# Optimization experiments

Measured on AMD Instinct MI355X. Metric: run time of the kernel, lower is better.

## Reference

```python
import jax, jax.numpy as jnp
import numpy as np

CUTOFF = 10.0
NUM_GAUSSIANS = 50
LOG2 = float(np.log(2.0))
PI = float(np.pi)


def ssp(v):
    # shifted softplus: softplus(x) - log(2)
    return jax.nn.softplus(v) - LOG2


def setup_inputs() -> dict:
    key = jax.random.key(0)
    ks = jax.random.split(key, 16)
    N, E, H, F, G, L = 10000, 320000, 128, 128, NUM_GAUSSIANS, 6
    s = 0.08  # param scale to keep activations stable over 6 layers
    return {
        "x": jax.random.randint(ks[0], (N,), 0, 100),
        "edge_index": jax.random.randint(ks[1], (2, E), 0, N),
        "edge_dist": jax.random.uniform(ks[2], (E,), jnp.float32) * CUTOFF,
        "emb": jax.random.normal(ks[3], (100, H), jnp.float32) * s,
        "mlp_w1": jax.random.normal(ks[4], (L, G, F), jnp.float32) * s,
        "mlp_b1": jnp.zeros((L, F), jnp.float32),
        "mlp_w2": jax.random.normal(ks[5], (L, F, F), jnp.float32) * s,
        "mlp_b2": jnp.zeros((L, F), jnp.float32),
        "lin1_w": jax.random.normal(ks[6], (L, H, F), jnp.float32) * s,
        "lin2_w": jax.random.normal(ks[7], (L, F, H), jnp.float32) * s,
        "lin2_b": jnp.zeros((L, H), jnp.float32),
        "lin_w": jax.random.normal(ks[8], (L, H, H), jnp.float32) * s,
        "lin_b": jnp.zeros((L, H), jnp.float32),
        "out1_w": jax.random.normal(ks[9], (H, H // 2), jnp.float32) * s,
        "out1_b": jnp.zeros((H // 2,), jnp.float32),
        "out2_w": jax.random.normal(ks[10], (H // 2, H // 2), jnp.float32) * s,
        "out2_b": jnp.zeros((H // 2,), jnp.float32),
        "ro_w": jax.random.normal(ks[11], (H // 2, 12), jnp.float32) * s,
        "ro_b": jnp.zeros((12,), jnp.float32),
    }


def reference(x, edge_index, edge_dist, emb, mlp_w1, mlp_b1, mlp_w2, mlp_b2,
              lin1_w, lin2_w, lin2_b, lin_w, lin_b,
              out1_w, out1_b, out2_w, out2_b, ro_w, ro_b):
    N = x.shape[0]
    L = mlp_w1.shape[0]
    src, dst = edge_index[0], edge_index[1]

    h = emb[x]  # [N, H]

    # Gaussian smearing of distances -> [E, G]
    offset = jnp.linspace(0.0, CUTOFF, NUM_GAUSSIANS)
    coeff = -0.5 / (offset[1] - offset[0]) ** 2
    ea = jnp.exp(coeff * (edge_dist[:, None] - offset[None, :]) ** 2)

    # cosine cutoff envelope C [E]
    C = 0.5 * (jnp.cos(edge_dist * PI / CUTOFF) + 1.0)

    for l in range(L):
        # per-edge filter: MLP(gaussian) * cutoff  -> [E, F]
        W = (ssp(ea @ mlp_w1[l] + mlp_b1[l]) @ mlp_w2[l] + mlp_b2[l]) * C[:, None]
        xf = h @ lin1_w[l]                      # [N, F] (lin1, no bias)
        msg = xf[src] * W                       # gather + elementwise [E, F]
        agg = jax.ops.segment_sum(msg, dst, num_segments=N)  # scatter-add
        conv = agg @ lin2_w[l] + lin2_b[l]      # [N, H]
        h = h + (ssp(conv) @ lin_w[l] + lin_b[l])

    t = ssp(h @ out1_w + out1_b)
    t = t @ out2_w + out2_b
    h_agg = jnp.sum(t, axis=0)                  # [H//2]
    return h_agg @ ro_w + ro_b                  # [12]
```

## Files before the change

kernel.cpp:

```cpp
#include <hip/hip_runtime.h>
#include <math.h>

#define E_NUM 320000
#define N_NUM 10000
#define NB16  (N_NUM / 16)
#define TAB   2048

typedef unsigned short ushort_t;
typedef short short8_t __attribute__((ext_vector_type(8)));
typedef float f32x4    __attribute__((ext_vector_type(4)));

#define WP_O1   294912
#define WP_O2   303104
#define WP_W1T  307200
#define WP_W2T  356352
#define WP_TOT  454656

#define HB  1250
#define PB  ((WP_TOT + 255) / 256)

#define FK_SC 625
#define FK_TB 768
#define FK_EM NB16

__device__ __forceinline__ float ssp_f(float x) {
    return fmaxf(x, 0.f) + __logf(1.f + __expf(-fabsf(x))) - 0.69314718056f;
}

__device__ __forceinline__ float bf2f(ushort_t u) {
    union { unsigned int i; float f; } v;
    v.i = ((unsigned int)u) << 16;
    return v.f;
}
__device__ __forceinline__ ushort_t f2bf(float f) {
    union { float f; unsigned int i; } v;
    v.f = f;
    unsigned int u = v.i;
    unsigned int r = (u + 0x7FFFu + ((u >> 16) & 1u)) >> 16;
    return (ushort_t)r;
}

__global__ __launch_bounds__(256) void hist_pack_kernel(const int* __restrict__ ei,
                                                        int* __restrict__ counts,
                                                        const float* __restrict__ lin2_w,
                                                        const float* __restrict__ lin_w,
                                                        const float* __restrict__ lin1_w,
                                                        const float* __restrict__ o1w,
                                                        const float* __restrict__ o2w,
                                                        const float* __restrict__ mlp_w1,
                                                        const float* __restrict__ mlp_w2,
                                                        short* __restrict__ wpack) {
    if (blockIdx.x < HB) {
        int e = blockIdx.x * 256 + threadIdx.x;
        atomicAdd(&counts[ei[E_NUM + e]], 1);
        return;
    }
    int idx = (blockIdx.x - HB) * 256 + threadIdx.x;
    const int M128 = 16384;
    if (idx < 18 * M128) {
        int g = idx / M128, r = idx % M128;
        const float* src;
        if (g < 6) src = lin2_w + g * M128;
        else if (g < 12) src = lin_w + (g - 6) * M128;
        else src = lin1_w + (g - 12) * M128;
        int j = r & 7, L = (r >> 3) & 63, ks = (r >> 9) & 3, t = r >> 11;
        int n = t * 16 + (L & 15);
        int k = ks * 32 + (L >> 4) * 8 + j;
        wpack[idx] = (short)f2bf(src[k * 128 + n]);
    } else if (idx < WP_O2) {
        int r = idx - WP_O1;
        int j = r & 7, L = (r >> 3) & 63, ks = (r >> 9) & 3, t = r >> 11;
        int n = t * 16 + (L & 15);
        int k = ks * 32 + (L >> 4) * 8 + j;
        wpack[idx] = (short)f2bf(o1w[k * 64 + n]);
    } else if (idx < WP_W1T) {
        int r = idx - WP_O2;
        int j = r & 7, L = (r >> 3) & 63, ks = (r >> 9) & 1, t = r >> 10;
        int n = t * 16 + (L & 15);
        int k = ks * 32 + (L >> 4) * 8 + j;
        wpack[idx] = (short)f2bf(o2w[k * 64 + n]);
    } else if (idx < WP_W1T + 6 * 8192 && idx >= WP_W1T) {
        int r2 = idx - WP_W1T;
        int g = r2 / 8192, r = r2 % 8192;
        int j = r & 7, L = (r >> 3) & 63, ks = (r >> 9) & 1, t = r >> 10;
        int n = t * 16 + (L & 15);
        int k = ks * 32 + (L >> 4) * 8 + j;
        float v = (k < 50) ? mlp_w1[g * 6400 + k * 128 + n] : 0.f;
        wpack[idx] = (short)f2bf(v);
    } else if (idx < WP_TOT) {
        int r2 = idx - WP_W2T;
        int g = r2 / M128, r = r2 % M128;
        int j = r & 7, L = (r >> 3) & 63, ks = (r >> 9) & 3, t = r >> 11;
        int n = t * 16 + (L & 15);
        int k = ks * 32 + (L >> 4) * 8 + j;
        wpack[idx] = (short)f2bf(mlp_w2[g * M128 + k * 128 + n]);
    }
}

__global__ __launch_bounds__(1024) void scan_kernel(const int* __restrict__ counts,
                                                    int* __restrict__ offs,
                                                    int* __restrict__ cursor) {
    __shared__ int part[1024];
    const int tid = threadIdx.x;
    const int CH = 10;
    int base = tid * CH;
    int s = 0;
    #pragma unroll
    for (int i = 0; i < CH; ++i) {
        int idx = base + i;
        if (idx < N_NUM) s += counts[idx];
    }
    part[tid] = s;
    __syncthreads();
    for (int off = 1; off < 1024; off <<= 1) {
        int v = (tid >= off) ? part[tid - off] : 0;
        __syncthreads();
        part[tid] += v;
        __syncthreads();
    }
    int run = (tid > 0) ? part[tid - 1] : 0;
    #pragma unroll
    for (int i = 0; i < CH; ++i) {
        int idx = base + i;
        if (idx < N_NUM) {
            offs[idx] = run;
            cursor[idx] = run;
            run += counts[idx];
        }
    }
    if (tid == 1023) offs[N_NUM] = part[1023];
}

__global__ __launch_bounds__(512) void front_kernel(const int* __restrict__ ei,
                                                    const float* __restrict__ dist,
                                                    int* __restrict__ cursor,
                                                    int* __restrict__ meta,
                                                    const short* __restrict__ w1t,
                                                    const float* __restrict__ mlp_b1,
                                                    const short* __restrict__ w2t,
                                                    const float* __restrict__ mlp_b2,
                                                    ushort_t* __restrict__ tabB,
                                                    const int* __restrict__ x,
                                                    const float* __restrict__ emb,
                                                    const short* __restrict__ w1p0,
                                                    float* __restrict__ h,
                                                    ushort_t* __restrict__ xf) {
    __shared__ short EA[16 * 72];
    __shared__ short HD[16 * 136];
    __shared__ int s_x[16];
    const int tid = threadIdx.x;

    if (blockIdx.x < FK_SC) {
        int e = blockIdx.x * 512 + tid;
        int d = ei[E_NUM + e];
        int pos = atomicAdd(&cursor[d], 1);
        float t = dist[e] * ((float)(TAB - 1) / 10.0f);
        int i0 = (int)(t + 0.5f);
        if (i0 > TAB - 1) i0 = TAB - 1;
        meta[pos] = (i0 << 14) | ei[e];
        return;
    }

    const int wv = tid >> 6;
    const int lane = tid & 63;
    const int m = lane & 15, q = lane >> 4;

    if (blockIdx.x < FK_SC + FK_TB) {
        const int bt = blockIdx.x - FK_SC;
        const int l = bt >> 7;
        const int r0 = (bt & 127) * 16;
        const float DG = 10.0f / (float)(TAB - 1);
        const float STEP = 10.0f / 49.0f;
        const float COEFF = -0.5f / (STEP * STEP);

        for (int i = tid; i < 16 * 64; i += 512) {
            int r = i >> 6, k = i & 63;
            float v = 0.f;
            if (k < 50) {
                float d = (float)(r0 + r) * DG;
                float t = d - (float)k * STEP;
                v = __expf(COEFF * t * t);
            }
            EA[r * 72 + k] = (short)f2bf(v);
        }
        __syncthreads();

        {
            f32x4 acc = {0.f, 0.f, 0.f, 0.f};
            #pragma unroll
            for (int ks = 0; ks < 2; ++ks) {
                short8_t a = *(const short8_t*)(EA + m * 72 + ks * 32 + q * 8);
                short8_t b = *(const short8_t*)(w1t + l * 8192 + (wv * 2 + ks) * 512 + lane * 8);
                acc = __builtin_amdgcn_mfma_f32_16x16x32_bf16(a, b, acc, 0, 0, 0);
            }
            float bv = mlp_b1[l * 128 + wv * 16 + m];
            #pragma unroll
            for (int i = 0; i < 4; ++i)
                HD[(q * 4 + i) * 136 + wv * 16 + m] = (short)f2bf(ssp_f(acc[i] + bv));
        }
        __syncthreads();

        {
            f32x4 acc = {0.f, 0.f, 0.f, 0.f};
            #pragma unroll
            for (int ks = 0; ks < 4; ++ks) {
                short8_t a = *(const short8_t*)(HD + m * 136 + ks * 32 + q * 8);
                short8_t b = *(const short8_t*)(w2t + l * 16384 + (wv * 4 + ks) * 512 + lane * 8);
                acc = __builtin_amdgcn_mfma_f32_16x16x32_bf16(a, b, acc, 0, 0, 0);
            }
            int col = wv * 16 + m;
            float bv = mlp_b2[l * 128 + col];
            ushort_t* tl = tabB + (size_t)l * TAB * 128;
            #pragma unroll
            for (int i = 0; i < 4; ++i) {
                int row = r0 + q * 4 + i;
                float d = (float)row * DG;
                float C = 0.5f * (__cosf(d * 0.31415926535f) + 1.0f);
                tl[(size_t)row * 128 + col] = f2bf((acc[i] + bv) * C);
            }
        }
        return;
    }

    {
        const int n0 = (blockIdx.x - FK_SC - FK_TB) * 16;
        if (tid < 16) s_x[tid] = x[n0 + tid];
        __syncthreads();
        {
            int r = tid >> 5;
            int c4 = (tid & 31) * 4;
            float4 v = *(const float4*)(emb + (size_t)s_x[r] * 128 + c4);
            *(float4*)(h + (size_t)(n0 + r) * 128 + c4) = v;
            short4 o;
            o.x = (short)f2bf(v.x); o.y = (short)f2bf(v.y);
            o.z = (short)f2bf(v.z); o.w = (short)f2bf(v.w);
            *(short4*)(HD + r * 136 + c4) = o;
        }
        __syncthreads();
        f32x4 acc = {0.f, 0.f, 0.f, 0.f};
        #pragma unroll
        for (int ks = 0; ks < 4; ++ks) {
            short8_t a = *(const short8_t*)(HD + m * 136 + ks * 32 + q * 8);
            short8_t b = *(const short8_t*)(w1p0 + (wv * 4 + ks) * 512 + lane * 8);
            acc = __builtin_amdgcn_mfma_f32_16x16x32_bf16(a, b, acc, 0, 0, 0);
        }
        #pragma unroll
        for (int i = 0; i < 4; ++i) {
            int grow = n0 + q * 4 + i;
            xf[(size_t)grow * 128 + wv * 16 + m] = f2bf(acc[i]);
        }
    }
}

__device__ __forceinline__ void nacc8(short8_t x, short8_t t, float* o) {
    #pragma unroll
    for (int j = 0; j < 8; ++j)
        o[j] = fmaf(bf2f((ushort_t)x[j]), bf2f((ushort_t)t[j]), o[j]);
}

template <bool LAST>
__global__ __launch_bounds__(512, 4) void layer_kernel(const int* __restrict__ offs,
                                                    const int* __restrict__ meta,
                                                    const ushort_t* __restrict__ xf,
                                                    const ushort_t* __restrict__ tabB,
                                                    const short* __restrict__ w2p,
                                                    const float* __restrict__ lin2_b,
                                                    const short* __restrict__ wlp,
                                                    const float* __restrict__ lin_b,
                                                    const short* __restrict__ w1p,
                                                    float* __restrict__ h,
                                                    ushort_t* __restrict__ xf_out,
                                                    const short* __restrict__ o1p,
                                                    const float* __restrict__ o1b,
                                                    const short* __restrict__ o2p,
                                                    const float* __restrict__ o2b,
                                                    float* __restrict__ gs) {
    __shared__ short A1[16 * 136];
    __shared__ short A2[16 * 136];
    __shared__ float P[16 * 128];
    __shared__ float red[4][64];
    const int tid = threadIdx.x;
    const int n0 = blockIdx.x * 16;
    const int wv = tid >> 6;
    const int lane = tid & 63;
    const int strm = wv >> 2;

    {
        const int qt = lane >> 4;
        const int c8 = (lane & 15) * 8;
        const int row = (wv & 3) * 4 + qt;
        const int node = n0 + row;
        int s0 = offs[node];
        int s1 = offs[node + 1];
        int mid = s0 + ((s1 - s0) >> 1);
        int e   = strm ? mid : s0;
        int end = strm ? s1  : mid;

        float accA[8] = {0.f, 0.f, 0.f, 0.f, 0.f, 0.f, 0.f, 0.f};
        float accB[8] = {0.f, 0.f, 0.f, 0.f, 0.f, 0.f, 0.f, 0.f};

        const int nb = (end - e) >> 2;
        if (nb > 0) {
            int mnxt[4] = {0, 0, 0, 0};
            short8_t xv[4], tv[4];
            {
                int mcur[4];
                #pragma unroll
                for (int u = 0; u < 4; ++u) mcur[u] = meta[e + u];
                if (nb > 1) {
                    #pragma unroll
                    for (int u = 0; u < 4; ++u) mnxt[u] = meta[e + 4 + u];
                }
                #pragma unroll
                for (int u = 0; u < 4; ++u) {
                    xv[u] = *(const short8_t*)(xf + (size_t)(mcur[u] & 0x3FFF) * 128 + c8);
                    tv[u] = *(const short8_t*)(tabB + (size_t)((unsigned)mcur[u] >> 14) * 128 + c8);
                }
            }
            for (int b = 0; b < nb - 1; ++b) {
                short8_t xn[4], tn[4];
                #pragma unroll
                for (int u = 0; u < 4; ++u) {
                    xn[u] = *(const short8_t*)(xf + (size_t)(mnxt[u] & 0x3FFF) * 128 + c8);
                    tn[u] = *(const short8_t*)(tabB + (size_t)((unsigned)mnxt[u] >> 14) * 128 + c8);
                }
                int mn2[4] = {0, 0, 0, 0};
                if (b + 2 < nb) {
                    #pragma unroll
                    for (int u = 0; u < 4; ++u) mn2[u] = meta[e + 4 * (b + 2) + u];
                }
                #pragma unroll
                for (int u = 0; u < 4; ++u)
                    nacc8(xv[u], tv[u], (u & 1) ? accB : accA);
                #pragma unroll
                for (int u = 0; u < 4; ++u) { xv[u] = xn[u]; tv[u] = tn[u]; mnxt[u] = mn2[u]; }
            }
            #pragma unroll
            for (int u = 0; u < 4; ++u)
                nacc8(xv[u], tv[u], (u & 1) ? accB : accA);
            e += nb * 4;
        }
        int rem = end - e;
        if (rem > 0) {
            int mm[4];
            #pragma unroll
            for (int u = 0; u < 4; ++u) mm[u] = meta[e + ((u < rem) ? u : 0)];
            short8_t xv[4], tv[4];
            #pragma unroll
            for (int u = 0; u < 4; ++u) {
                xv[u] = *(const short8_t*)(xf + (size_t)(mm[u] & 0x3FFF) * 128 + c8);
                tv[u] = *(const short8_t*)(tabB + (size_t)((unsigned)mm[u] >> 14) * 128 + c8);
            }
            #pragma unroll
            for (int u = 0; u < 4; ++u)
                if (u < rem) nacc8(xv[u], tv[u], (u & 1) ? accB : accA);
        }

        if (!strm) {
            #pragma unroll
            for (int j = 0; j < 8; ++j)
                P[row * 128 + c8 + j] = accA[j] + accB[j];
        }
        __syncthreads();
        if (strm) {
            short8_t out;
            #pragma unroll
            for (int j = 0; j < 8; ++j)
                out[j] = (short)f2bf(accA[j] + accB[j] + P[row * 128 + c8 + j]);
            *(short8_t*)&A1[row * 136 + c8] = out;
        }
    }
    __syncthreads();

    const int m = lane & 15, q = lane >> 4;
    const int t = wv;

    {
        f32x4 acc = {0.f, 0.f, 0.f, 0.f};
        #pragma unroll
        for (int ks = 0; ks < 4; ++ks) {
            short8_t a = *(const short8_t*)(A1 + m * 136 + ks * 32 + q * 8);
            short8_t b = *(const short8_t*)(w2p + (t * 4 + ks) * 512 + lane * 8);
            acc = __builtin_amdgcn_mfma_f32_16x16x32_bf16(a, b, acc, 0, 0, 0);
        }
        float bv = lin2_b[t * 16 + m];
        #pragma unroll
        for (int i = 0; i < 4; ++i)
            A2[(q * 4 + i) * 136 + t * 16 + m] = (short)f2bf(ssp_f(acc[i] + bv));
    }
    __syncthreads();

    {
        f32x4 acc = {0.f, 0.f, 0.f, 0.f};
        #pragma unroll
        for (int ks = 0; ks < 4; ++ks) {
            short8_t a = *(const short8_t*)(A2 + m * 136 + ks * 32 + q * 8);
            short8_t b = *(const short8_t*)(wlp + (t * 4 + ks) * 512 + lane * 8);
            acc = __builtin_amdgcn_mfma_f32_16x16x32_bf16(a, b, acc, 0, 0, 0);
        }
        float bv = lin_b[t * 16 + m];
        #pragma unroll
        for (int i = 0; i < 4; ++i) {
            int r = q * 4 + i;
            int grow = n0 + r;
            float h0 = h[(size_t)grow * 128 + t * 16 + m];
            float hn = h0 + acc[i] + bv;
            if (!LAST) h[(size_t)grow * 128 + t * 16 + m] = hn;
            A1[r * 136 + t * 16 + m] = (short)f2bf(hn);
        }
    }
    __syncthreads();

    if constexpr (!LAST) {
        f32x4 acc = {0.f, 0.f, 0.f, 0.f};
        #pragma unroll
        for (int ks = 0; ks < 4; ++ks) {
            short8_t a = *(const short8_t*)(A1 + m * 136 + ks * 32 + q * 8);
            short8_t b = *(const short8_t*)(w1p + (t * 4 + ks) * 512 + lane * 8);
            acc = __builtin_amdgcn_mfma_f32_16x16x32_bf16(a, b, acc, 0, 0, 0);
        }
        #pragma unroll
        for (int i = 0; i < 4; ++i) {
            int r = q * 4 + i;
            int grow = n0 + r;
            xf_out[(size_t)grow * 128 + t * 16 + m] = f2bf(acc[i]);
        }
    } else {
        if (wv < 4) {
            f32x4 acc = {0.f, 0.f, 0.f, 0.f};
            #pragma unroll
            for (int ks = 0; ks < 4; ++ks) {
                short8_t a = *(const short8_t*)(A1 + m * 136 + ks * 32 + q * 8);
                short8_t b = *(const short8_t*)(o1p + (wv * 4 + ks) * 512 + lane * 8);
                acc = __builtin_amdgcn_mfma_f32_16x16x32_bf16(a, b, acc, 0, 0, 0);
            }
            float bv = o1b[wv * 16 + m];
            #pragma unroll
            for (int i = 0; i < 4; ++i) {
                int r = q * 4 + i;
                A2[r * 136 + wv * 16 + m] = (short)f2bf(ssp_f(acc[i] + bv));
            }
        }
        __syncthreads();
        if (wv < 4) {
            f32x4 acc = {0.f, 0.f, 0.f, 0.f};
            #pragma unroll
            for (int ks = 0; ks < 2; ++ks) {
                short8_t a = *(const short8_t*)(A2 + m * 136 + ks * 32 + q * 8);
                short8_t b = *(const short8_t*)(o2p + (wv * 2 + ks) * 512 + lane * 8);
                acc = __builtin_amdgcn_mfma_f32_16x16x32_bf16(a, b, acc, 0, 0, 0);
            }
            float bv = o2b[wv * 16 + m];
            float part = acc[0] + acc[1] + acc[2] + acc[3] + 4.0f * bv;
            red[q][wv * 16 + m] = part;
        }
        __syncthreads();
        if (tid < 64) {
            float s = red[0][tid] + red[1][tid] + red[2][tid] + red[3][tid];
            atomicAdd(&gs[tid], s);
        }
    }
}

__global__ void final_kernel(const float* __restrict__ gs,
                             const float* __restrict__ ro_w,
                             const float* __restrict__ ro_b,
                             float* __restrict__ out) {
    int i = threadIdx.x;
    if (i < 12) {
        float s = ro_b[i];
        for (int k = 0; k < 64; ++k) s = fmaf(gs[k], ro_w[k * 12 + i], s);
        out[i] = s;
    }
}

extern "C" void kernel_launch(void* const* d_in, const int* in_sizes, int n_in,
                              void* d_out, int out_size, void* d_ws, size_t ws_size,
                              hipStream_t stream) {
    const int*   x      = (const int*)d_in[0];
    const int*   ei     = (const int*)d_in[1];
    const float* dist   = (const float*)d_in[2];
    const float* emb    = (const float*)d_in[3];
    const float* mlp_w1 = (const float*)d_in[4];
    const float* mlp_b1 = (const float*)d_in[5];
    const float* mlp_w2 = (const float*)d_in[6];
    const float* mlp_b2 = (const float*)d_in[7];
    const float* lin1_w = (const float*)d_in[8];
    const float* lin2_w = (const float*)d_in[9];
    const float* lin2_b = (const float*)d_in[10];
    const float* lin_w  = (const float*)d_in[11];
    const float* lin_b  = (const float*)d_in[12];
    const float* out1_w = (const float*)d_in[13];
    const float* out1_b = (const float*)d_in[14];
    const float* out2_w = (const float*)d_in[15];
    const float* out2_b = (const float*)d_in[16];
    const float* ro_w   = (const float*)d_in[17];
    const float* ro_b   = (const float*)d_in[18];
    float* out = (float*)d_out;

    char* base = (char*)d_ws;
    float*    h     = (float*)base;     base += (size_t)N_NUM * 128 * 4;
    ushort_t* tabB  = (ushort_t*)base;  base += (size_t)6 * TAB * 128 * 2;
    ushort_t* xf0   = (ushort_t*)base;  base += (size_t)N_NUM * 128 * 2;
    ushort_t* xf1   = (ushort_t*)base;  base += (size_t)N_NUM * 128 * 2;
    int*      meta  = (int*)base;       base += (size_t)E_NUM * 4;
    short*    wpack = (short*)base;     base += (size_t)WP_TOT * 2;
    float*    gs    = (float*)base;     base += 64 * 4;
    int*      offs  = (int*)base;       base += (N_NUM + 1) * 4;
    int*      cursor= (int*)base;       base += N_NUM * 4;
    int*      counts= (int*)base;       base += N_NUM * 4;

    hipMemsetAsync(counts, 0, N_NUM * sizeof(int), stream);
    hipMemsetAsync(gs, 0, 64 * sizeof(float), stream);

    hist_pack_kernel<<<HB + PB, 256, 0, stream>>>(
        ei, counts, lin2_w, lin_w, lin1_w, out1_w, out2_w, mlp_w1, mlp_w2, wpack);

    scan_kernel<<<1, 1024, 0, stream>>>(counts, offs, cursor);

    front_kernel<<<FK_SC + FK_TB + FK_EM, 512, 0, stream>>>(
        ei, dist, cursor, meta,
        wpack + WP_W1T, mlp_b1, wpack + WP_W2T, mlp_b2, tabB,
        x, emb, wpack + 12 * 16384, h, xf0);

    const short* o1p = wpack + WP_O1;
    const short* o2p = wpack + WP_O2;

    for (int l = 0; l < 6; ++l) {
        ushort_t* xin  = (l & 1) ? xf1 : xf0;
        ushort_t* xout = (l & 1) ? xf0 : xf1;
        const ushort_t* tl = tabB + (size_t)l * TAB * 128;
        const short* w2p = wpack + l * 16384;
        const short* wlp = wpack + (6 + l) * 16384;
        if (l < 5) {
            const short* w1p = wpack + (12 + l + 1) * 16384;
            layer_kernel<false><<<NB16, 512, 0, stream>>>(
                offs, meta, xin, tl,
                w2p, lin2_b + l * 128, wlp, lin_b + l * 128, w1p,
                h, xout, nullptr, nullptr, nullptr, nullptr, nullptr);
        } else {
            layer_kernel<true><<<NB16, 512, 0, stream>>>(
                offs, meta, xin, tl,
                w2p, lin2_b + l * 128, wlp, lin_b + l * 128, nullptr,
                h, nullptr, o1p, out1_b, o2p, out2_b, gs);
        }
    }

    final_kernel<<<1, 64, 0, stream>>>(gs, ro_w, ro_b, out);
}
```

Measured before the change: 289.6 us.

## Fuse all stages into one persistent cooperative kernel with grid syncs

Replaces the sequence of separate launches (histogram/pack, scan, front, six layer kernels) with one cooperative persistent kernel. Stages are separated by grid.sync, and blocks loop over tiles with a grid capped at 512 blocks. The aim is to remove per-launch overhead and inter-kernel gaps. In exchange, occupancy is limited to co-resident blocks, the scan runs on a single block, and each layer needs a grid-wide barrier. The old multi-kernel path remains as a fallback.

```diff
diff --git a/kernel.cpp b/kernel.cpp
--- a/kernel.cpp
+++ b/kernel.cpp
@@ -1,10 +1,14 @@
 #include <hip/hip_runtime.h>
+#include <hip/hip_cooperative_groups.h>
 #include <math.h>
+
+namespace cg = cooperative_groups;
 
 #define E_NUM 320000
 #define N_NUM 10000
 #define NB16  (N_NUM / 16)
 #define TAB   2048
+#define BT    512
 
 typedef unsigned short ushort_t;
 typedef short short8_t __attribute__((ext_vector_type(8)));
@@ -18,7 +22,6 @@
 
 #define HB  1250
 #define PB  ((WP_TOT + 255) / 256)
-
 #define FK_SC 625
 #define FK_TB 768
 #define FK_EM NB16
@@ -40,22 +43,21 @@
     return (ushort_t)r;
 }
 
-__global__ __launch_bounds__(256) void hist_pack_kernel(const int* __restrict__ ei,
-                                                        int* __restrict__ counts,
-                                                        const float* __restrict__ lin2_w,
-                                                        const float* __restrict__ lin_w,
-                                                        const float* __restrict__ lin1_w,
-                                                        const float* __restrict__ o1w,
-                                                        const float* __restrict__ o2w,
-                                                        const float* __restrict__ mlp_w1,
-                                                        const float* __restrict__ mlp_w2,
-                                                        short* __restrict__ wpack) {
-    if (blockIdx.x < HB) {
-        int e = blockIdx.x * 256 + threadIdx.x;
-        atomicAdd(&counts[ei[E_NUM + e]], 1);
-        return;
-    }
-    int idx = (blockIdx.x - HB) * 256 + threadIdx.x;
+__device__ __forceinline__ void nacc8(short8_t x, short8_t t, float* o) {
+    #pragma unroll
+    for (int j = 0; j < 8; ++j)
+        o[j] = fmaf(bf2f((ushort_t)x[j]), bf2f((ushort_t)t[j]), o[j]);
+}
+
+__device__ __forceinline__ void pack_one(int idx,
+                                         const float* __restrict__ lin2_w,
+                                         const float* __restrict__ lin_w,
+                                         const float* __restrict__ lin1_w,
+                                         const float* __restrict__ o1w,
+                                         const float* __restrict__ o2w,
+                                         const float* __restrict__ mlp_w1,
+                                         const float* __restrict__ mlp_w2,
+                                         short* __restrict__ wpack) {
     const int M128 = 16384;
     if (idx < 18 * M128) {
         int g = idx / M128, r = idx % M128;
@@ -79,7 +81,7 @@
         int n = t * 16 + (L & 15);
         int k = ks * 32 + (L >> 4) * 8 + j;
         wpack[idx] = (short)f2bf(o2w[k * 64 + n]);
-    } else if (idx < WP_W1T + 6 * 8192 && idx >= WP_W1T) {
+    } else if (idx < WP_W2T) {
         int r2 = idx - WP_W1T;
         int g = r2 / 8192, r = r2 % 8192;
         int j = r & 7, L = (r >> 3) & 63, ks = (r >> 9) & 1, t = r >> 10;
@@ -95,6 +97,399 @@
         int k = ks * 32 + (L >> 4) * 8 + j;
         wpack[idx] = (short)f2bf(mlp_w2[g * M128 + k * 128 + n]);
     }
+}
+
+__global__ __launch_bounds__(512, 4) void mega_kernel(
+    const int* __restrict__ x, const int* __restrict__ ei,
+    const float* __restrict__ dist, const float* __restrict__ emb,
+    const float* __restrict__ mlp_w1, const float* __restrict__ mlp_b1,
+    const float* __restrict__ mlp_w2, const float* __restrict__ mlp_b2,
+    const float* __restrict__ lin1_w, const float* __restrict__ lin2_w,
+    const float* __restrict__ lin2_b, const float* __restrict__ lin_w,
+    const float* __restrict__ lin_b, const float* __restrict__ o1w,
+    const float* __restrict__ o1b, const float* __restrict__ o2w,
+    const float* __restrict__ o2b, const float* __restrict__ ro_w,
+    const float* __restrict__ ro_b,
+    float* __restrict__ h, ushort_t* __restrict__ tabB,
+    ushort_t* __restrict__ xf0, ushort_t* __restrict__ xf1,
+    int* __restrict__ meta, short* __restrict__ wpack,
+    float* __restrict__ gs, int* __restrict__ offs,
+    int* __restrict__ cursor, int* __restrict__ counts,
+    float* __restrict__ out)
+{
+    cg::grid_group grid = cg::this_grid();
+    __shared__ short EA[16 * 72];
+    __shared__ short HD[16 * 136];
+    __shared__ short A2s[16 * 136];
+    __shared__ float P[16 * 128];
+    __shared__ float red[4][64];
+    __shared__ int s_x[16];
+    const int tid  = threadIdx.x;
+    const int bid  = blockIdx.x;
+    const int nblk = gridDim.x;
+    const int gsz  = nblk * BT;
+    const int gtid = bid * BT + tid;
+    const int wv   = tid >> 6;
+    const int lane = tid & 63;
+    const int m    = lane & 15, q = lane >> 4;
+
+    for (int i = gtid; i < N_NUM; i += gsz) counts[i] = 0;
+    if (gtid < 64) gs[gtid] = 0.f;
+    grid.sync();
+
+    for (int e = gtid; e < E_NUM; e += gsz) atomicAdd(&counts[ei[E_NUM + e]], 1);
+    for (int idx = gtid; idx < WP_TOT; idx += gsz)
+        pack_one(idx, lin2_w, lin_w, lin1_w, o1w, o2w, mlp_w1, mlp_w2, wpack);
+    grid.sync();
+
+    if (bid == 0) {
+        int* part = (int*)P;
+        const int CH = 20;
+        int base = tid * CH;
+        int s = 0;
+        #pragma unroll
+        for (int i = 0; i < CH; ++i) {
+            int idx = base + i;
+            if (idx < N_NUM) s += counts[idx];
+        }
+        part[tid] = s;
+        __syncthreads();
+        for (int off = 1; off < 512; off <<= 1) {
+            int v = (tid >= off) ? part[tid - off] : 0;
+            __syncthreads();
+            part[tid] += v;
+            __syncthreads();
+        }
+        int run = (tid > 0) ? part[tid - 1] : 0;
+        #pragma unroll
+        for (int i = 0; i < CH; ++i) {
+            int idx = base + i;
+            if (idx < N_NUM) {
+                offs[idx] = run;
+                cursor[idx] = run;
+                run += counts[idx];
+            }
+        }
+        if (tid == 511) offs[N_NUM] = part[511];
+    }
+    grid.sync();
+
+    for (int e = gtid; e < E_NUM; e += gsz) {
+        int d = ei[E_NUM + e];
+        int pos = atomicAdd(&cursor[d], 1);
+        float t = dist[e] * ((float)(TAB - 1) / 10.0f);
+        int i0 = (int)(t + 0.5f);
+        if (i0 > TAB - 1) i0 = TAB - 1;
+        meta[pos] = (i0 << 14) | ei[e];
+    }
+
+    {
+        const short* w1t = wpack + WP_W1T;
+        const short* w2t = wpack + WP_W2T;
+        const float DG = 10.0f / (float)(TAB - 1);
+        const float STEP = 10.0f / 49.0f;
+        const float COEFF = -0.5f / (STEP * STEP);
+        for (int bt2 = bid; bt2 < 768; bt2 += nblk) {
+            __syncthreads();
+            const int l = bt2 >> 7;
+            const int r0 = (bt2 & 127) * 16;
+            for (int i = tid; i < 16 * 64; i += BT) {
+                int r = i >> 6, k = i & 63;
+                float v = 0.f;
+                if (k < 50) {
+                    float d = (float)(r0 + r) * DG;
+                    float t = d - (float)k * STEP;
+                    v = __expf(COEFF * t * t);
+                }
+                EA[r * 72 + k] = (short)f2bf(v);
+            }
+            __syncthreads();
+            {
+                f32x4 acc = {0.f, 0.f, 0.f, 0.f};
+                #pragma unroll
+                for (int ks = 0; ks < 2; ++ks) {
+                    short8_t a = *(const short8_t*)(EA + m * 72 + ks * 32 + q * 8);
+                    short8_t b = *(const short8_t*)(w1t + l * 8192 + (wv * 2 + ks) * 512 + lane * 8);
+                    acc = __builtin_amdgcn_mfma_f32_16x16x32_bf16(a, b, acc, 0, 0, 0);
+                }
+                float bv = mlp_b1[l * 128 + wv * 16 + m];
+                #pragma unroll
+                for (int i = 0; i < 4; ++i)
+                    HD[(q * 4 + i) * 136 + wv * 16 + m] = (short)f2bf(ssp_f(acc[i] + bv));
+            }
+            __syncthreads();
+            {
+                f32x4 acc = {0.f, 0.f, 0.f, 0.f};
+                #pragma unroll
+                for (int ks = 0; ks < 4; ++ks) {
+                    short8_t a = *(const short8_t*)(HD + m * 136 + ks * 32 + q * 8);
+                    short8_t b = *(const short8_t*)(w2t + l * 16384 + (wv * 4 + ks) * 512 + lane * 8);
+                    acc = __builtin_amdgcn_mfma_f32_16x16x32_bf16(a, b, acc, 0, 0, 0);
+                }
+                int col = wv * 16 + m;
+                float bv = mlp_b2[l * 128 + col];
+                ushort_t* tl = tabB + (size_t)l * TAB * 128;
+                #pragma unroll
+                for (int i = 0; i < 4; ++i) {
+                    int row = r0 + q * 4 + i;
+                    float d = (float)row * DG;
+                    float C = 0.5f * (__cosf(d * 0.31415926535f) + 1.0f);
+                    tl[(size_t)row * 128 + col] = f2bf((acc[i] + bv) * C);
+                }
+            }
+        }
+    }
+
+    {
+        const short* w1p0 = wpack + 12 * 16384;
+        for (int nt = bid; nt < 625; nt += nblk) {
+            __syncthreads();
+            const int n0 = nt * 16;
+            if (tid < 16) s_x[tid] = x[n0 + tid];
+            __syncthreads();
+            {
+                int r = tid >> 5;
+                int c4 = (tid & 31) * 4;
+                float4 v = *(const float4*)(emb + (size_t)s_x[r] * 128 + c4);
+                *(float4*)(h + (size_t)(n0 + r) * 128 + c4) = v;
+                short4 o;
+                o.x = (short)f2bf(v.x); o.y = (short)f2bf(v.y);
+                o.z = (short)f2bf(v.z); o.w = (short)f2bf(v.w);
+                *(short4*)(HD + r * 136 + c4) = o;
+            }
+            __syncthreads();
+            f32x4 acc = {0.f, 0.f, 0.f, 0.f};
+            #pragma unroll
+            for (int ks = 0; ks < 4; ++ks) {
+                short8_t a = *(const short8_t*)(HD + m * 136 + ks * 32 + q * 8);
+                short8_t b = *(const short8_t*)(w1p0 + (wv * 4 + ks) * 512 + lane * 8);
+                acc = __builtin_amdgcn_mfma_f32_16x16x32_bf16(a, b, acc, 0, 0, 0);
+            }
+            #pragma unroll
+            for (int i = 0; i < 4; ++i) {
+                int grow = n0 + q * 4 + i;
+                xf0[(size_t)grow * 128 + wv * 16 + m] = f2bf(acc[i]);
+            }
+        }
+    }
+    grid.sync();
+
+    const short* o1p = wpack + WP_O1;
+    const short* o2p = wpack + WP_O2;
+    for (int l = 0; l < 6; ++l) {
+        const ushort_t* xin = (l & 1) ? xf1 : xf0;
+        ushort_t* xout      = (l & 1) ? xf0 : xf1;
+        const ushort_t* tl  = tabB + (size_t)l * TAB * 128;
+        const short* w2p = wpack + l * 16384;
+        const short* wlp = wpack + (6 + l) * 16384;
+        const short* w1p = wpack + (12 + ((l + 1 < 6) ? (l + 1) : 0)) * 16384;
+        const bool last = (l == 5);
+
+        for (int nt = bid; nt < 625; nt += nblk) {
+            __syncthreads();
+            const int n0 = nt * 16;
+            const int strm = wv >> 2;
+
+            {
+                const int qt = lane >> 4;
+                const int c8 = (lane & 15) * 8;
+                const int row = (wv & 3) * 4 + qt;
+                const int node = n0 + row;
+                int s0 = offs[node];
+                int s1 = offs[node + 1];
+                int mid = s0 + ((s1 - s0) >> 1);
+                int e   = strm ? mid : s0;
+                int end = strm ? s1  : mid;
+
+                float accA[8] = {0.f, 0.f, 0.f, 0.f, 0.f, 0.f, 0.f, 0.f};
+                float accB[8] = {0.f, 0.f, 0.f, 0.f, 0.f, 0.f, 0.f, 0.f};
+
+                const int nb = (end - e) >> 2;
+                if (nb > 0) {
+                    int mnxt[4] = {0, 0, 0, 0};
+                    short8_t xv[4], tv[4];
+                    {
+                        int mcur[4];
+                        #pragma unroll
+                        for (int u = 0; u < 4; ++u) mcur[u] = meta[e + u];
+                        if (nb > 1) {
+                            #pragma unroll
+                            for (int u = 0; u < 4; ++u) mnxt[u] = meta[e + 4 + u];
+                        }
+                        #pragma unroll
+                        for (int u = 0; u < 4; ++u) {
+                            xv[u] = *(const short8_t*)(xin + (size_t)(mcur[u] & 0x3FFF) * 128 + c8);
+                            tv[u] = *(const short8_t*)(tl + (size_t)((unsigned)mcur[u] >> 14) * 128 + c8);
+                        }
+                    }
+                    for (int b = 0; b < nb - 1; ++b) {
+                        short8_t xn[4], tn[4];
+                        #pragma unroll
+                        for (int u = 0; u < 4; ++u) {
+                            xn[u] = *(const short8_t*)(xin + (size_t)(mnxt[u] & 0x3FFF) * 128 + c8);
+                            tn[u] = *(const short8_t*)(tl + (size_t)((unsigned)mnxt[u] >> 14) * 128 + c8);
+                        }
+                        int mn2[4] = {0, 0, 0, 0};
+                        if (b + 2 < nb) {
+                            #pragma unroll
+                            for (int u = 0; u < 4; ++u) mn2[u] = meta[e + 4 * (b + 2) + u];
+                        }
+                        #pragma unroll
+                        for (int u = 0; u < 4; ++u)
+                            nacc8(xv[u], tv[u], (u & 1) ? accB : accA);
+                        #pragma unroll
+                        for (int u = 0; u < 4; ++u) { xv[u] = xn[u]; tv[u] = tn[u]; mnxt[u] = mn2[u]; }
+                    }
+                    #pragma unroll
+                    for (int u = 0; u < 4; ++u)
+                        nacc8(xv[u], tv[u], (u & 1) ? accB : accA);
+                    e += nb * 4;
+                }
+                int rem = end - e;
+                if (rem > 0) {
+                    int mm[4];
+                    #pragma unroll
+                    for (int u = 0; u < 4; ++u) mm[u] = meta[e + ((u < rem) ? u : 0)];
+                    short8_t xv[4], tv[4];
+                    #pragma unroll
+                    for (int u = 0; u < 4; ++u) {
+                        xv[u] = *(const short8_t*)(xin + (size_t)(mm[u] & 0x3FFF) * 128 + c8);
+                        tv[u] = *(const short8_t*)(tl + (size_t)((unsigned)mm[u] >> 14) * 128 + c8);
+                    }
+                    #pragma unroll
+                    for (int u = 0; u < 4; ++u)
+                        if (u < rem) nacc8(xv[u], tv[u], (u & 1) ? accB : accA);
+                }
+
+                if (!strm) {
+                    #pragma unroll
+                    for (int j = 0; j < 8; ++j)
+                        P[row * 128 + c8 + j] = accA[j] + accB[j];
+                }
+                __syncthreads();
+                if (strm) {
+                    short8_t o;
+                    #pragma unroll
+                    for (int j = 0; j < 8; ++j)
+                        o[j] = (short)f2bf(accA[j] + accB[j] + P[row * 128 + c8 + j]);
+                    *(short8_t*)&HD[row * 136 + c8] = o;
+                }
+            }
+            __syncthreads();
+
+            const int t = wv;
+
+            {
+                f32x4 acc = {0.f, 0.f, 0.f, 0.f};
+                #pragma unroll
+                for (int ks = 0; ks < 4; ++ks) {
+                    short8_t a = *(const short8_t*)(HD + m * 136 + ks * 32 + q * 8);
+                    short8_t b = *(const short8_t*)(w2p + (t * 4 + ks) * 512 + lane * 8);
+                    acc = __builtin_amdgcn_mfma_f32_16x16x32_bf16(a, b, acc, 0, 0, 0);
+                }
+                float bv = lin2_b[l * 128 + t * 16 + m];
+                #pragma unroll
+                for (int i = 0; i < 4; ++i)
+                    A2s[(q * 4 + i) * 136 + t * 16 + m] = (short)f2bf(ssp_f(acc[i] + bv));
+            }
+            __syncthreads();
+
+            {
+                f32x4 acc = {0.f, 0.f, 0.f, 0.f};
+                #pragma unroll
+                for (int ks = 0; ks < 4; ++ks) {
+                    short8_t a = *(const short8_t*)(A2s + m * 136 + ks * 32 + q * 8);
+                    short8_t b = *(const short8_t*)(wlp + (t * 4 + ks) * 512 + lane * 8);
+                    acc = __builtin_amdgcn_mfma_f32_16x16x32_bf16(a, b, acc, 0, 0, 0);
+                }
+                float bv = lin_b[l * 128 + t * 16 + m];
+                #pragma unroll
+                for (int i = 0; i < 4; ++i) {
+                    int r = q * 4 + i;
+                    int grow = n0 + r;
+                    float h0 = h[(size_t)grow * 128 + t * 16 + m];
+                    float hn = h0 + acc[i] + bv;
+                    if (!last) h[(size_t)grow * 128 + t * 16 + m] = hn;
+                    HD[r * 136 + t * 16 + m] = (short)f2bf(hn);
+                }
+            }
+            __syncthreads();
+
+            if (!last) {
+                f32x4 acc = {0.f, 0.f, 0.f, 0.f};
+                #pragma unroll
+                for (int ks = 0; ks < 4; ++ks) {
+                    short8_t a = *(const short8_t*)(HD + m * 136 + ks * 32 + q * 8);
+                    short8_t b = *(const short8_t*)(w1p + (t * 4 + ks) * 512 + lane * 8);
+                    acc = __builtin_amdgcn_mfma_f32_16x16x32_bf16(a, b, acc, 0, 0, 0);
+                }
+                #pragma unroll
+                for (int i = 0; i < 4; ++i) {
+                    int r = q * 4 + i;
+                    int grow = n0 + r;
+                    xout[(size_t)grow * 128 + t * 16 + m] = f2bf(acc[i]);
+                }
+            } else {
+                if (wv < 4) {
+                    f32x4 acc = {0.f, 0.f, 0.f, 0.f};
+                    #pragma unroll
+                    for (int ks = 0; ks < 4; ++ks) {
+                        short8_t a = *(const short8_t*)(HD + m * 136 + ks * 32 + q * 8);
+                        short8_t b = *(const short8_t*)(o1p + (wv * 4 + ks) * 512 + lane * 8);
+                        acc = __builtin_amdgcn_mfma_f32_16x16x32_bf16(a, b, acc, 0, 0, 0);
+                    }
+                    float bv = o1b[wv * 16 + m];
+                    #pragma unroll
+                    for (int i = 0; i < 4; ++i)
+                        A2s[(q * 4 + i) * 136 + wv * 16 + m] = (short)f2bf(ssp_f(acc[i] + bv));
+                }
+                __syncthreads();
+                if (wv < 4) {
+                    f32x4 acc = {0.f, 0.f, 0.f, 0.f};
+                    #pragma unroll
+                    for (int ks = 0; ks < 2; ++ks) {
+                        short8_t a = *(const short8_t*)(A2s + m * 136 + ks * 32 + q * 8);
+                        short8_t b = *(const short8_t*)(o2p + (wv * 2 + ks) * 512 + lane * 8);
+                        acc = __builtin_amdgcn_mfma_f32_16x16x32_bf16(a, b, acc, 0, 0, 0);
+                    }
+                    float bv = o2b[wv * 16 + m];
+                    float part = acc[0] + acc[1] + acc[2] + acc[3] + 4.0f * bv;
+                    red[q][wv * 16 + m] = part;
+                }
+                __syncthreads();
+                if (tid < 64) {
+                    float s = red[0][tid] + red[1][tid] + red[2][tid] + red[3][tid];
+                    atomicAdd(&gs[tid], s);
+                }
+            }
+        }
+        grid.sync();
+    }
+
+    if (bid == 0 && tid < 12) {
+        float s = ro_b[tid];
+        for (int k = 0; k < 64; ++k) s = fmaf(gs[k], ro_w[k * 12 + tid], s);
+        out[tid] = s;
+    }
+}
+
+__global__ __launch_bounds__(256) void hist_pack_kernel(const int* __restrict__ ei,
+                                                        int* __restrict__ counts,
+                                                        const float* __restrict__ lin2_w,
+                                                        const float* __restrict__ lin_w,
+                                                        const float* __restrict__ lin1_w,
+                                                        const float* __restrict__ o1w,
+                                                        const float* __restrict__ o2w,
+                                                        const float* __restrict__ mlp_w1,
+                                                        const float* __restrict__ mlp_w2,
+                                                        short* __restrict__ wpack) {
+    if (blockIdx.x < HB) {
+        int e = blockIdx.x * 256 + threadIdx.x;
+        atomicAdd(&counts[ei[E_NUM + e]], 1);
+        return;
+    }
+    int idx = (blockIdx.x - HB) * 256 + threadIdx.x;
+    pack_one(idx, lin2_w, lin_w, lin1_w, o1w, o2w, mlp_w1, mlp_w2, wpack);
 }
 
 __global__ __launch_bounds__(1024) void scan_kernel(const int* __restrict__ counts,
@@ -184,7 +579,6 @@
             EA[r * 72 + k] = (short)f2bf(v);
         }
         __syncthreads();
-
         {
             f32x4 acc = {0.f, 0.f, 0.f, 0.f};
             #pragma unroll
@@ -199,7 +593,6 @@
                 HD[(q * 4 + i) * 136 + wv * 16 + m] = (short)f2bf(ssp_f(acc[i] + bv));
         }
         __syncthreads();
-
         {
             f32x4 acc = {0.f, 0.f, 0.f, 0.f};
             #pragma unroll
@@ -250,12 +643,6 @@
             xf[(size_t)grow * 128 + wv * 16 + m] = f2bf(acc[i]);
         }
     }
-}
-
-__device__ __forceinline__ void nacc8(short8_t x, short8_t t, float* o) {
-    #pragma unroll
-    for (int j = 0; j < 8; ++j)
-        o[j] = fmaf(bf2f((ushort_t)x[j]), bf2f((ushort_t)t[j]), o[j]);
 }
 
 template <bool LAST>
@@ -510,14 +897,34 @@
     int*      cursor= (int*)base;       base += N_NUM * 4;
     int*      counts= (int*)base;       base += N_NUM * 4;
 
+    void* args[] = {
+        (void*)&x, (void*)&ei, (void*)&dist, (void*)&emb,
+        (void*)&mlp_w1, (void*)&mlp_b1, (void*)&mlp_w2, (void*)&mlp_b2,
+        (void*)&lin1_w, (void*)&lin2_w, (void*)&lin2_b, (void*)&lin_w,
+        (void*)&lin_b, (void*)&out1_w, (void*)&out1_b, (void*)&out2_w,
+        (void*)&out2_b, (void*)&ro_w, (void*)&ro_b,
+        (void*)&h, (void*)&tabB, (void*)&xf0, (void*)&xf1,
+        (void*)&meta, (void*)&wpack, (void*)&gs, (void*)&offs,
+        (void*)&cursor, (void*)&counts, (void*)&out
+    };
+    hipError_t lerr = hipErrorUnknown;
+    int maxPerCU = 0;
+    hipError_t qerr = hipOccupancyMaxActiveBlocksPerMultiprocessor(
+        &maxPerCU, mega_kernel, BT, 0);
+    if (qerr == hipSuccess && maxPerCU >= 1) {
+        int grid = maxPerCU * 256;
+        if (grid > 512) grid = 512;
+        lerr = hipLaunchCooperativeKernel((void*)mega_kernel, dim3(grid), dim3(BT),
+                                          args, 0, stream);
+    }
+    if (lerr == hipSuccess) return;
+
     hipMemsetAsync(counts, 0, N_NUM * sizeof(int), stream);
     hipMemsetAsync(gs, 0, 64 * sizeof(float), stream);
 
     hist_pack_kernel<<<HB + PB, 256, 0, stream>>>(
         ei, counts, lin2_w, lin_w, lin1_w, out1_w, out2_w, mlp_w1, mlp_w2, wpack);
-
     scan_kernel<<<1, 1024, 0, stream>>>(counts, offs, cursor);
-
     front_kernel<<<FK_SC + FK_TB + FK_EM, 512, 0, stream>>>(
         ei, dist, cursor, meta,
         wpack + WP_W1T, mlp_b1, wpack + WP_W2T, mlp_b2, tabB,
```

Measured after the change: 670.3 us. 131% more time.

## Shrink filter table to 160 rows in LDS with linear interpolation

Applied to the files above, without the earlier changes.

Replaces the 2048-row per-layer bf16 filter table held in global memory with a 160-row table that each layer block copies into shared memory. Per edge, the two neighbouring rows are read from LDS and linearly interpolated using a 10-bit fraction packed into the edge metadata. This removes one global gather per edge and shrinks table construction work. The cost is extra ALU for the interpolation, a per-block table load, larger LDS use, and an accuracy change from interpolating a coarse table. Launch bounds are relaxed from a minimum of 4 blocks per CU to the default.

```diff
diff --git a/kernel.cpp b/kernel.cpp
--- a/kernel.cpp
+++ b/kernel.cpp
@@ -4,7 +4,8 @@
 #define E_NUM 320000
 #define N_NUM 10000
 #define NB16  (N_NUM / 16)
-#define TAB   2048
+#define TS_ROWS 160
+#define TS_STR  136
 
 typedef unsigned short ushort_t;
 typedef short short8_t __attribute__((ext_vector_type(8)));
@@ -20,7 +21,7 @@
 #define PB  ((WP_TOT + 255) / 256)
 
 #define FK_SC 625
-#define FK_TB 768
+#define FK_TB 60
 #define FK_EM NB16
 
 __device__ __forceinline__ float ssp_f(float x) {
@@ -79,7 +80,7 @@
         int n = t * 16 + (L & 15);
         int k = ks * 32 + (L >> 4) * 8 + j;
         wpack[idx] = (short)f2bf(o2w[k * 64 + n]);
-    } else if (idx < WP_W1T + 6 * 8192 && idx >= WP_W1T) {
+    } else if (idx < WP_W2T) {
         int r2 = idx - WP_W1T;
         int g = r2 / 8192, r = r2 % 8192;
         int j = r & 7, L = (r >> 3) & 63, ks = (r >> 9) & 1, t = r >> 10;
@@ -139,7 +140,7 @@
                                                     const float* __restrict__ mlp_b1,
                                                     const short* __restrict__ w2t,
                                                     const float* __restrict__ mlp_b2,
-                                                    ushort_t* __restrict__ tabB,
+                                                    ushort_t* __restrict__ tabS,
                                                     const int* __restrict__ x,
                                                     const float* __restrict__ emb,
                                                     const short* __restrict__ w1p0,
@@ -154,10 +155,13 @@
         int e = blockIdx.x * 512 + tid;
         int d = ei[E_NUM + e];
         int pos = atomicAdd(&cursor[d], 1);
-        float t = dist[e] * ((float)(TAB - 1) / 10.0f);
-        int i0 = (int)(t + 0.5f);
-        if (i0 > TAB - 1) i0 = TAB - 1;
-        meta[pos] = (i0 << 14) | ei[e];
+        float t = dist[e] * ((float)(TS_ROWS - 1) / 10.0f);
+        int i0 = (int)t;
+        if (i0 > TS_ROWS - 2) i0 = TS_ROWS - 2;
+        float fr = t - (float)i0;
+        int fq = (int)(fr * 1024.0f + 0.5f);
+        if (fq > 1023) fq = 1023;
+        meta[pos] = (fq << 22) | (i0 << 14) | ei[e];
         return;
     }
 
@@ -167,9 +171,9 @@
 
     if (blockIdx.x < FK_SC + FK_TB) {
         const int bt = blockIdx.x - FK_SC;
-        const int l = bt >> 7;
-        const int r0 = (bt & 127) * 16;
-        const float DG = 10.0f / (float)(TAB - 1);
+        const int l = bt / 10;
+        const int r0 = (bt % 10) * 16;
+        const float DG = 10.0f / (float)(TS_ROWS - 1);
         const float STEP = 10.0f / 49.0f;
         const float COEFF = -0.5f / (STEP * STEP);
 
@@ -210,7 +214,7 @@
             }
             int col = wv * 16 + m;
             float bv = mlp_b2[l * 128 + col];
-            ushort_t* tl = tabB + (size_t)l * TAB * 128;
+            ushort_t* tl = tabS + (size_t)l * TS_ROWS * 128;
             #pragma unroll
             for (int i = 0; i < 4; ++i) {
                 int row = r0 + q * 4 + i;
@@ -252,17 +256,26 @@
     }
 }
 
-__device__ __forceinline__ void nacc8(short8_t x, short8_t t, float* o) {
+__device__ __forceinline__ void lerp_acc(short8_t x, const short* TS, int mm,
+                                         int c8, float* o) {
+    int i0 = (mm >> 14) & 0xFF;
+    float fr = (float)((unsigned)mm >> 22) * (1.0f / 1024.0f);
+    short8_t t0 = *(const short8_t*)(TS + i0 * TS_STR + c8);
+    short8_t t1 = *(const short8_t*)(TS + i0 * TS_STR + TS_STR + c8);
     #pragma unroll
-    for (int j = 0; j < 8; ++j)
-        o[j] = fmaf(bf2f((ushort_t)x[j]), bf2f((ushort_t)t[j]), o[j]);
+    for (int j = 0; j < 8; ++j) {
+        float a = bf2f((ushort_t)t0[j]);
+        float b = bf2f((ushort_t)t1[j]);
+        float w = fmaf(fr, b - a, a);
+        o[j] = fmaf(bf2f((ushort_t)x[j]), w, o[j]);
+    }
 }
 
 template <bool LAST>
-__global__ __launch_bounds__(512, 4) void layer_kernel(const int* __restrict__ offs,
+__global__ __launch_bounds__(512) void layer_kernel(const int* __restrict__ offs,
                                                     const int* __restrict__ meta,
                                                     const ushort_t* __restrict__ xf,
-                                                    const ushort_t* __restrict__ tabB,
+                                                    const ushort_t* __restrict__ tabS,
                                                     const short* __restrict__ w2p,
                                                     const float* __restrict__ lin2_b,
                                                     const short* __restrict__ wlp,
@@ -275,6 +288,7 @@
                                                     const short* __restrict__ o2p,
                                                     const float* __restrict__ o2b,
                                                     float* __restrict__ gs) {
+    __shared__ short TS[TS_ROWS * TS_STR];
     __shared__ short A1[16 * 136];
     __shared__ short A2[16 * 136];
     __shared__ float P[16 * 128];
@@ -284,6 +298,13 @@
     const int wv = tid >> 6;
     const int lane = tid & 63;
     const int strm = wv >> 2;
+
+    for (int i = tid; i < TS_ROWS * 16; i += 512) {
+        int r = i >> 4, c8 = (i & 15) * 8;
+        *(short8_t*)&TS[r * TS_STR + c8] =
+            *(const short8_t*)(tabS + (size_t)r * 128 + c8);
+    }
+    __syncthreads();
 
     {
         const int qt = lane >> 4;
@@ -301,29 +322,23 @@
 
         const int nb = (end - e) >> 2;
         if (nb > 0) {
-            int mnxt[4] = {0, 0, 0, 0};
-            short8_t xv[4], tv[4];
-            {
-                int mcur[4];
+            int mcur[4], mnxt[4] = {0, 0, 0, 0};
+            short8_t xv[4];
+            #pragma unroll
+            for (int u = 0; u < 4; ++u) mcur[u] = meta[e + u];
+            if (nb > 1) {
                 #pragma unroll
-                for (int u = 0; u < 4; ++u) mcur[u] = meta[e + u];
-                if (nb > 1) {
-                    #pragma unroll
-                    for (int u = 0; u < 4; ++u) mnxt[u] = meta[e + 4 + u];
-                }
+                for (int u = 0; u < 4; ++u) mnxt[u] = meta[e + 4 + u];
+            }
+            #pragma unroll
+            for (int u = 0; u < 4; ++u)
+                xv[u] = *(const short8_t*)(xf + (size_t)(mcur[u] & 0x3FFF) * 128 + c8);
+
+            for (int b = 0; b < nb - 1; ++b) {
+                short8_t xn[4];
                 #pragma unroll
-                for (int u = 0; u < 4; ++u) {
-                    xv[u] = *(const short8_t*)(xf + (size_t)(mcur[u] & 0x3FFF) * 128 + c8);
-                    tv[u] = *(const short8_t*)(tabB + (size_t)((unsigned)mcur[u] >> 14) * 128 + c8);
-                }
-            }
-            for (int b = 0; b < nb - 1; ++b) {
-                short8_t xn[4], tn[4];
-                #pragma unroll
-                for (int u = 0; u < 4; ++u) {
+                for (int u = 0; u < 4; ++u)
                     xn[u] = *(const short8_t*)(xf + (size_t)(mnxt[u] & 0x3FFF) * 128 + c8);
-                    tn[u] = *(const short8_t*)(tabB + (size_t)((unsigned)mnxt[u] >> 14) * 128 + c8);
-                }
                 int mn2[4] = {0, 0, 0, 0};
                 if (b + 2 < nb) {
                     #pragma unroll
@@ -331,13 +346,15 @@
                 }
                 #pragma unroll
                 for (int u = 0; u < 4; ++u)
-                    nacc8(xv[u], tv[u], (u & 1) ? accB : accA);
+                    lerp_acc(xv[u], TS, mcur[u], c8, (u & 1) ? accB : accA);
                 #pragma unroll
-                for (int u = 0; u < 4; ++u) { xv[u] = xn[u]; tv[u] = tn[u]; mnxt[u] = mn2[u]; }
+                for (int u = 0; u < 4; ++u) {
+                    xv[u] = xn[u]; mcur[u] = mnxt[u]; mnxt[u] = mn2[u];
+                }
             }
             #pragma unroll
             for (int u = 0; u < 4; ++u)
-                nacc8(xv[u], tv[u], (u & 1) ? accB : accA);
+                lerp_acc(xv[u], TS, mcur[u], c8, (u & 1) ? accB : accA);
             e += nb * 4;
         }
         int rem = end - e;
@@ -345,15 +362,13 @@
             int mm[4];
             #pragma unroll
             for (int u = 0; u < 4; ++u) mm[u] = meta[e + ((u < rem) ? u : 0)];
-            short8_t xv[4], tv[4];
-            #pragma unroll
-            for (int u = 0; u < 4; ++u) {
+            short8_t xv[4];
+            #pragma unroll
+            for (int u = 0; u < 4; ++u)
                 xv[u] = *(const short8_t*)(xf + (size_t)(mm[u] & 0x3FFF) * 128 + c8);
-                tv[u] = *(const short8_t*)(tabB + (size_t)((unsigned)mm[u] >> 14) * 128 + c8);
-            }
             #pragma unroll
             for (int u = 0; u < 4; ++u)
-                if (u < rem) nacc8(xv[u], tv[u], (u & 1) ? accB : accA);
+                if (u < rem) lerp_acc(xv[u], TS, mm[u], c8, (u & 1) ? accB : accA);
         }
 
         if (!strm) {
@@ -500,7 +515,7 @@
 
     char* base = (char*)d_ws;
     float*    h     = (float*)base;     base += (size_t)N_NUM * 128 * 4;
-    ushort_t* tabB  = (ushort_t*)base;  base += (size_t)6 * TAB * 128 * 2;
+    ushort_t* tabS  = (ushort_t*)base;  base += (size_t)6 * TS_ROWS * 128 * 2;
     ushort_t* xf0   = (ushort_t*)base;  base += (size_t)N_NUM * 128 * 2;
     ushort_t* xf1   = (ushort_t*)base;  base += (size_t)N_NUM * 128 * 2;
     int*      meta  = (int*)base;       base += (size_t)E_NUM * 4;
@@ -520,7 +535,7 @@
 
     front_kernel<<<FK_SC + FK_TB + FK_EM, 512, 0, stream>>>(
         ei, dist, cursor, meta,
-        wpack + WP_W1T, mlp_b1, wpack + WP_W2T, mlp_b2, tabB,
+        wpack + WP_W1T, mlp_b1, wpack + WP_W2T, mlp_b2, tabS,
         x, emb, wpack + 12 * 16384, h, xf0);
 
     const short* o1p = wpack + WP_O1;
@@ -529,7 +544,7 @@
     for (int l = 0; l < 6; ++l) {
         ushort_t* xin  = (l & 1) ? xf1 : xf0;
         ushort_t* xout = (l & 1) ? xf0 : xf1;
-        const ushort_t* tl = tabB + (size_t)l * TAB * 128;
+        const ushort_t* tl = tabS + (size_t)l * TS_ROWS * 128;
         const short* w2p = wpack + l * 16384;
         const short* wlp = wpack + (6 + l) * 16384;
         if (l < 5) {
```

After: 299.3 us. 3.3% more time.
